# Kernel optimization log

Hardware: AMD Instinct MI355X
Metric: run time of the kernel (lower is better)

Reference implementation:

```python
import jax, jax.numpy as jnp
import numpy as np
from functools import partial

B, T, H, W, CIN, F = 8, 16, 64, 64, 32, 32
K = 3
BN_EPS = 1e-3


def _conv(x, w):
    # x: [N,H,W,Cin], w: [kh,kw,Cin,Cout], SAME padding, stride 1
    return jax.lax.conv_general_dilated(
        x, w, window_strides=(1, 1), padding='SAME',
        dimension_numbers=('NHWC', 'HWIO', 'NHWC'))


def _hard_sigmoid(x):
    # Keras hard_sigmoid: clip(0.2*x + 0.5, 0, 1)
    return jnp.clip(0.2 * x + 0.5, 0.0, 1.0)


def setup_inputs() -> dict:
    key = jax.random.key(0)
    ks = jax.random.split(key, 4)
    x = jax.random.normal(ks[0], (B, T, H, W, CIN), dtype=jnp.float32)
    Wx = jax.random.normal(ks[1], (K, K, CIN, 4 * F), dtype=jnp.float32) * 0.05
    Wh = jax.random.normal(ks[2], (K, K, F, 4 * F), dtype=jnp.float32) * 0.05
    b = jnp.zeros((4 * F,), dtype=jnp.float32)
    gamma = jnp.ones((F,), dtype=jnp.float32)
    beta = jnp.zeros((F,), dtype=jnp.float32)
    moving_mean = jnp.zeros((F,), dtype=jnp.float32)
    moving_var = jnp.ones((F,), dtype=jnp.float32)
    return {"x": x, "Wx": Wx, "Wh": Wh, "b": b, "gamma": gamma,
            "beta": beta, "moving_mean": moving_mean, "moving_var": moving_var}


def _conv_lstm(x, Wx, Wh, b):
    # Precompute input-to-gate convs for all timesteps at once: [B*T,H,W,4F]
    xg = _conv(x.reshape(B * T, H, W, CIN), Wx) + b
    xg = xg.reshape(B, T, H, W, 4 * F).transpose(1, 0, 2, 3, 4)  # [T,B,H,W,4F]

    def step(carry, xg_t):
        h, c = carry
        g = xg_t + _conv(h, Wh)  # [B,H,W,4F]
        i, f, cc, o = jnp.split(g, 4, axis=-1)  # Keras gate order i,f,c,o
        i = _hard_sigmoid(i)
        f = _hard_sigmoid(f)
        o = _hard_sigmoid(o)
        c = f * c + i * jnp.tanh(cc)
        h = o * jnp.tanh(c)
        return (h, c), h

    h0 = jnp.zeros((B, H, W, F), dtype=x.dtype)
    c0 = jnp.zeros((B, H, W, F), dtype=x.dtype)
    _, hs = jax.lax.scan(step, (h0, c0), xg)  # hs: [T,B,H,W,F]
    return hs.transpose(1, 0, 2, 3, 4)  # [B,T,H,W,F]


def reference(x, Wx, Wh, b, gamma, beta, moving_mean, moving_var):
    y = _conv_lstm(x, Wx, Wh, b)
    # BatchNorm in inference mode (training=False): use moving stats, eps=1e-3
    inv = gamma * jax.lax.rsqrt(moving_var + BN_EPS)
    return y * inv + (beta - moving_mean * inv)
```

## Files before the change

kernel.cpp:

```cpp
#include <hip/hip_runtime.h>
#include <math.h>

#define PSTR 40
#define GSTR 35
#define GPL  (64 * GSTR)

typedef _Float16 half8 __attribute__((ext_vector_type(8)));
typedef float    f32x4 __attribute__((ext_vector_type(4)));

__device__ __forceinline__ float fast_tanh(float v) {
    float e = __expf(2.f * v);
    return 1.f - 2.f / (e + 1.f);
}
__device__ __forceinline__ float hsig(float v) {
    return fminf(fmaxf(0.2f * v + 0.5f, 0.f), 1.f);
}

__global__ void prep_w(const float* __restrict__ Wx, const float* __restrict__ Wh,
                       _Float16* __restrict__ Wcx, _Float16* __restrict__ Wch) {
    const int k = blockIdx.x;
    const int n = threadIdx.x;
    const int tap = k >> 6, ci = k & 63;
    if (ci < 32) Wcx[(tap * 128 + n) * 32 + ci]        = (_Float16)Wx[(tap * 32 + ci) * 128 + n];
    else         Wch[(tap * 128 + n) * 32 + (ci - 32)] = (_Float16)Wh[(tap * 32 + (ci - 32)) * 128 + n];
}

__global__ __launch_bounds__(256, 2)
void lstm_step_k(const float* __restrict__ x, const _Float16* __restrict__ Wcx,
                 const _Float16* __restrict__ Wch, const float* __restrict__ bias,
                 const float* __restrict__ gamma_, const float* __restrict__ beta_,
                 const float* __restrict__ mmean, const float* __restrict__ mvar,
                 const _Float16* __restrict__ hprev, _Float16* __restrict__ hnext,
                 float* __restrict__ csw, float* __restrict__ out, int t)
{
    __shared__ _Float16 xp[100 * PSTR];
    __shared__ _Float16 hp[100 * PSTR];
    __shared__ float    glds[4 * GPL];

    const int tid  = threadIdx.x;
    const int lane = tid & 63;
    const int w    = tid >> 6;
    const int l15  = lane & 15, quad = lane >> 4;
    const int b = blockIdx.x, tx = blockIdx.y, ty = blockIdx.z;
    const int px0 = tx * 8, py0 = ty * 8;
    const int tile = ty * 8 + tx;

    const float* xt = x + (((size_t)b * 16 + t) * 4096) * 32;
    for (int i = tid; i < 400; i += 256) {
        const int pos = i >> 2, q = i & 3;
        const int row = pos / 10, col = pos - row * 10;
        const int gy = py0 + row - 1, gx = px0 + col - 1;
        half8 hv = {0, 0, 0, 0, 0, 0, 0, 0};
        if ((unsigned)gy < 64u && (unsigned)gx < 64u) {
            const float* s = xt + ((size_t)(gy * 64 + gx)) * 32 + q * 8;
            const float4 v0 = *(const float4*)s;
            const float4 v1 = *(const float4*)(s + 4);
            hv = (half8){(_Float16)v0.x, (_Float16)v0.y, (_Float16)v0.z, (_Float16)v0.w,
                         (_Float16)v1.x, (_Float16)v1.y, (_Float16)v1.z, (_Float16)v1.w};
        }
        *(half8*)&xp[pos * PSTR + q * 8] = hv;
    }
    if (t > 0) {
        const _Float16* hb = hprev + (size_t)b * 4096 * 32;
        for (int i = tid; i < 400; i += 256) {
            const int pos = i >> 2, q = i & 3;
            const int row = pos / 10, col = pos - row * 10;
            const int gy = py0 + row - 1, gx = px0 + col - 1;
            half8 hv = {0, 0, 0, 0, 0, 0, 0, 0};
            if ((unsigned)gy < 64u && (unsigned)gx < 64u)
                hv = *(const half8*)(hb + ((size_t)(gy * 64 + gx)) * 32 + q * 8);
            *(half8*)&hp[pos * PSTR + q * 8] = hv;
        }
    }

    const float bi0 = bias[w * 32 + l15];
    const float bi1 = bias[w * 32 + 16 + l15];

    __syncthreads();

    f32x4 acc[4][2];
    #pragma unroll
    for (int mt = 0; mt < 4; ++mt) {
        acc[mt][0] = (f32x4){bi0, bi0, bi0, bi0};
        acc[mt][1] = (f32x4){bi1, bi1, bi1, bi1};
    }

    int pb[4];
    #pragma unroll
    for (int mt = 0; mt < 4; ++mt) {
        const int p = mt * 16 + l15;
        pb[mt] = ((mt * 2 + (l15 >> 3)) * 10 + (l15 & 7)) * PSTR + quad * 8;
    }
    const _Float16* wbx = Wcx + ((size_t)(w * 32 + l15)) * 32 + quad * 8;
    const _Float16* wbh = Wch + ((size_t)(w * 32 + l15)) * 32 + quad * 8;

    #pragma unroll
    for (int tap = 0; tap < 9; ++tap) {
        const int ky = tap / 3, kx = tap - ky * 3;
        const int toff = (ky * 10 + kx) * PSTR;
        half8 a[4];
        #pragma unroll
        for (int mt = 0; mt < 4; ++mt) a[mt] = *(const half8*)&xp[pb[mt] + toff];
        #pragma unroll
        for (int ntl = 0; ntl < 2; ++ntl) {
            const half8 bf = *(const half8*)(wbx + tap * 4096 + ntl * 512);
            #pragma unroll
            for (int mt = 0; mt < 4; ++mt)
                acc[mt][ntl] = __builtin_amdgcn_mfma_f32_16x16x32_f16(a[mt], bf, acc[mt][ntl], 0, 0, 0);
        }
    }
    if (t > 0) {
        #pragma unroll
        for (int tap = 0; tap < 9; ++tap) {
            const int ky = tap / 3, kx = tap - ky * 3;
            const int toff = (ky * 10 + kx) * PSTR;
            half8 a[4];
            #pragma unroll
            for (int mt = 0; mt < 4; ++mt) a[mt] = *(const half8*)&hp[pb[mt] + toff];
            #pragma unroll
            for (int ntl = 0; ntl < 2; ++ntl) {
                const half8 bf = *(const half8*)(wbh + tap * 4096 + ntl * 512);
                #pragma unroll
                for (int mt = 0; mt < 4; ++mt)
                    acc[mt][ntl] = __builtin_amdgcn_mfma_f32_16x16x32_f16(a[mt], bf, acc[mt][ntl], 0, 0, 0);
            }
        }
    }

    #pragma unroll
    for (int mt = 0; mt < 4; ++mt)
        #pragma unroll
        for (int ntl = 0; ntl < 2; ++ntl)
            #pragma unroll
            for (int r = 0; r < 4; ++r) {
                const int px = mt * 16 + quad * 4 + r;
                glds[w * GPL + px * GSTR + ntl * 16 + l15] = acc[mt][ntl][r];
            }

    __syncthreads();

    const int pxt = tid >> 2, f0 = (tid & 3) * 8;
    const int gy = py0 + (pxt >> 3), gx = px0 + (pxt & 7);

    float gav[8], bev[8], mmv[8], mvv[8];
    *(float4*)&gav[0] = *(const float4*)&gamma_[f0];
    *(float4*)&gav[4] = *(const float4*)&gamma_[f0 + 4];
    *(float4*)&bev[0] = *(const float4*)&beta_[f0];
    *(float4*)&bev[4] = *(const float4*)&beta_[f0 + 4];
    *(float4*)&mmv[0] = *(const float4*)&mmean[f0];
    *(float4*)&mmv[4] = *(const float4*)&mmean[f0 + 4];
    *(float4*)&mvv[0] = *(const float4*)&mvar[f0];
    *(float4*)&mvv[4] = *(const float4*)&mvar[f0 + 4];

    float* cp = csw + (((size_t)b * 64 + tile) * 256 + tid) * 8;
    float cov[8];
    #pragma unroll
    for (int j = 0; j < 8; ++j) cov[j] = 0.f;
    if (t > 0) {
        *(f32x4*)&cov[0] = *(const f32x4*)cp;
        *(f32x4*)&cov[4] = *(const f32x4*)(cp + 4);
    }

    const int gb = pxt * GSTR + f0;
    half8 hv8;
    float ov[8], cnv[8];
    #pragma unroll
    for (int j = 0; j < 8; ++j) {
        const float gi = glds[0 * GPL + gb + j];
        const float gf = glds[1 * GPL + gb + j];
        const float gc = glds[2 * GPL + gb + j];
        const float go = glds[3 * GPL + gb + j];
        const float inv = gav[j] * rsqrtf(mvv[j] + 1e-3f);
        const float bnb = bev[j] - mmv[j] * inv;
        const float cn = hsig(gf) * cov[j] + hsig(gi) * fast_tanh(gc);
        const float hh = hsig(go) * fast_tanh(cn);
        cnv[j] = cn;
        hv8[j] = (_Float16)hh;
        ov[j] = hh * inv + bnb;
    }

    const size_t pix = ((size_t)(gy * 64 + gx)) * 32 + f0;
    _Float16* hq = hnext + (size_t)b * 4096 * 32;
    float* oq = out + (((size_t)b * 16 + t) * 4096) * 32;
    *(half8*)(hq + pix) = hv8;
    *(float4*)(oq + pix)     = *(float4*)&ov[0];
    *(float4*)(oq + pix + 4) = *(float4*)&ov[4];
    *(f32x4*)cp       = *(f32x4*)&cnv[0];
    *(f32x4*)(cp + 4) = *(f32x4*)&cnv[4];
}

extern "C" void kernel_launch(void* const* d_in, const int* in_sizes, int n_in,
                              void* d_out, int out_size, void* d_ws, size_t ws_size,
                              hipStream_t stream)
{
    const float* x      = (const float*)d_in[0];
    const float* Wx     = (const float*)d_in[1];
    const float* Wh     = (const float*)d_in[2];
    const float* bias   = (const float*)d_in[3];
    const float* gamma_ = (const float*)d_in[4];
    const float* beta_  = (const float*)d_in[5];
    const float* mmean  = (const float*)d_in[6];
    const float* mvar   = (const float*)d_in[7];
    float* out = (float*)d_out;

    char* wsb = (char*)d_ws;
    _Float16* h0  = (_Float16*)(wsb);
    _Float16* h1  = (_Float16*)(wsb + (1 << 21));
    float*    csw = (float*)(wsb + (1 << 22));
    _Float16* Wcx = (_Float16*)(wsb + (1 << 23));
    _Float16* Wch = (_Float16*)(wsb + (1 << 23) + 73728);

    prep_w<<<dim3(576), dim3(128), 0, stream>>>(Wx, Wh, Wcx, Wch);

    _Float16* hpr = h0;
    _Float16* hnx = h1;
    for (int t = 0; t < 16; ++t) {
        lstm_step_k<<<dim3(8, 8, 8), 256, 0, stream>>>(
            x, Wcx, Wch, bias, gamma_, beta_, mmean, mvar, hpr, hnx, csw, out, t);
        _Float16* tmp = hpr; hpr = hnx; hnx = tmp;
    }
}
```

Before: 293.0 us.

## Pre-convert x to fp16 and load conv operands directly from global memory

Adds a prep kernel that converts all of x to fp16 once, so each step reads half-precision input. The shared-memory halo staging and its barrier are dropped; every lane now loads its MFMA A-fragments straight from global memory (relying on L1/L2 caches) with per-tap bounds checks. The cell-state load is moved earlier to overlap with compute, and the h/c writes are skipped on the last timestep. The trade-off is 9x redundant global loads per tap and an extra full pass over x, in exchange for less LDS traffic, no staging barrier and higher potential occupancy.

```diff
diff --git a/kernel.cpp b/kernel.cpp
--- a/kernel.cpp
+++ b/kernel.cpp
@@ -1,7 +1,6 @@
 #include <hip/hip_runtime.h>
 #include <math.h>
 
-#define PSTR 40
 #define GSTR 35
 #define GPL  (64 * GSTR)
 
@@ -25,17 +24,24 @@
     else         Wch[(tap * 128 + n) * 32 + (ci - 32)] = (_Float16)Wh[(tap * 32 + (ci - 32)) * 128 + n];
 }
 
+__global__ __launch_bounds__(256)
+void prep_x(const float* __restrict__ x, _Float16* __restrict__ x16) {
+    const size_t i = ((size_t)blockIdx.x * 256 + threadIdx.x) * 8;
+    const float4 v0 = *(const float4*)(x + i);
+    const float4 v1 = *(const float4*)(x + i + 4);
+    *(half8*)(x16 + i) = (half8){(_Float16)v0.x, (_Float16)v0.y, (_Float16)v0.z, (_Float16)v0.w,
+                                 (_Float16)v1.x, (_Float16)v1.y, (_Float16)v1.z, (_Float16)v1.w};
+}
+
 __global__ __launch_bounds__(256, 2)
-void lstm_step_k(const float* __restrict__ x, const _Float16* __restrict__ Wcx,
+void lstm_step_k(const _Float16* __restrict__ x16, const _Float16* __restrict__ Wcx,
                  const _Float16* __restrict__ Wch, const float* __restrict__ bias,
                  const float* __restrict__ gamma_, const float* __restrict__ beta_,
                  const float* __restrict__ mmean, const float* __restrict__ mvar,
                  const _Float16* __restrict__ hprev, _Float16* __restrict__ hnext,
                  float* __restrict__ csw, float* __restrict__ out, int t)
 {
-    __shared__ _Float16 xp[100 * PSTR];
-    __shared__ _Float16 hp[100 * PSTR];
-    __shared__ float    glds[4 * GPL];
+    __shared__ float glds[4 * GPL];
 
     const int tid  = threadIdx.x;
     const int lane = tid & 63;
@@ -45,38 +51,25 @@
     const int px0 = tx * 8, py0 = ty * 8;
     const int tile = ty * 8 + tx;
 
-    const float* xt = x + (((size_t)b * 16 + t) * 4096) * 32;
-    for (int i = tid; i < 400; i += 256) {
-        const int pos = i >> 2, q = i & 3;
-        const int row = pos / 10, col = pos - row * 10;
-        const int gy = py0 + row - 1, gx = px0 + col - 1;
-        half8 hv = {0, 0, 0, 0, 0, 0, 0, 0};
-        if ((unsigned)gy < 64u && (unsigned)gx < 64u) {
-            const float* s = xt + ((size_t)(gy * 64 + gx)) * 32 + q * 8;
-            const float4 v0 = *(const float4*)s;
-            const float4 v1 = *(const float4*)(s + 4);
-            hv = (half8){(_Float16)v0.x, (_Float16)v0.y, (_Float16)v0.z, (_Float16)v0.w,
-                         (_Float16)v1.x, (_Float16)v1.y, (_Float16)v1.z, (_Float16)v1.w};
-        }
-        *(half8*)&xp[pos * PSTR + q * 8] = hv;
-    }
+    const int c0 = l15 & 7;
+    int rowm[4];
+    #pragma unroll
+    for (int mt = 0; mt < 4; ++mt) rowm[mt] = mt * 2 + (l15 >> 3);
+
+    const _Float16* xb = x16 + ((size_t)(b * 16 + t) * 4096) * 32;
+    const _Float16* hb = hprev + (size_t)b * 4096 * 32;
+
+    float* cp = csw + (((size_t)b * 64 + tile) * 256 + tid) * 8;
+    float cov[8];
+    #pragma unroll
+    for (int j = 0; j < 8; ++j) cov[j] = 0.f;
     if (t > 0) {
-        const _Float16* hb = hprev + (size_t)b * 4096 * 32;
-        for (int i = tid; i < 400; i += 256) {
-            const int pos = i >> 2, q = i & 3;
-            const int row = pos / 10, col = pos - row * 10;
-            const int gy = py0 + row - 1, gx = px0 + col - 1;
-            half8 hv = {0, 0, 0, 0, 0, 0, 0, 0};
-            if ((unsigned)gy < 64u && (unsigned)gx < 64u)
-                hv = *(const half8*)(hb + ((size_t)(gy * 64 + gx)) * 32 + q * 8);
-            *(half8*)&hp[pos * PSTR + q * 8] = hv;
-        }
+        *(f32x4*)&cov[0] = *(const f32x4*)cp;
+        *(f32x4*)&cov[4] = *(const f32x4*)(cp + 4);
     }
 
     const float bi0 = bias[w * 32 + l15];
     const float bi1 = bias[w * 32 + 16 + l15];
-
-    __syncthreads();
 
     f32x4 acc[4][2];
     #pragma unroll
@@ -85,22 +78,22 @@
         acc[mt][1] = (f32x4){bi1, bi1, bi1, bi1};
     }
 
-    int pb[4];
-    #pragma unroll
-    for (int mt = 0; mt < 4; ++mt) {
-        const int p = mt * 16 + l15;
-        pb[mt] = ((mt * 2 + (l15 >> 3)) * 10 + (l15 & 7)) * PSTR + quad * 8;
-    }
     const _Float16* wbx = Wcx + ((size_t)(w * 32 + l15)) * 32 + quad * 8;
     const _Float16* wbh = Wch + ((size_t)(w * 32 + l15)) * 32 + quad * 8;
 
     #pragma unroll
     for (int tap = 0; tap < 9; ++tap) {
         const int ky = tap / 3, kx = tap - ky * 3;
-        const int toff = (ky * 10 + kx) * PSTR;
+        const int gx = px0 + c0 + kx - 1;
+        const bool vx = (unsigned)gx < 64u;
         half8 a[4];
         #pragma unroll
-        for (int mt = 0; mt < 4; ++mt) a[mt] = *(const half8*)&xp[pb[mt] + toff];
+        for (int mt = 0; mt < 4; ++mt) {
+            const int gy = py0 + rowm[mt] + ky - 1;
+            a[mt] = (half8){0, 0, 0, 0, 0, 0, 0, 0};
+            if (vx && (unsigned)gy < 64u)
+                a[mt] = *(const half8*)(xb + ((size_t)(gy * 64 + gx)) * 32 + quad * 8);
+        }
         #pragma unroll
         for (int ntl = 0; ntl < 2; ++ntl) {
             const half8 bf = *(const half8*)(wbx + tap * 4096 + ntl * 512);
@@ -113,10 +106,16 @@
         #pragma unroll
         for (int tap = 0; tap < 9; ++tap) {
             const int ky = tap / 3, kx = tap - ky * 3;
-            const int toff = (ky * 10 + kx) * PSTR;
+            const int gx = px0 + c0 + kx - 1;
+            const bool vx = (unsigned)gx < 64u;
             half8 a[4];
             #pragma unroll
-            for (int mt = 0; mt < 4; ++mt) a[mt] = *(const half8*)&hp[pb[mt] + toff];
+            for (int mt = 0; mt < 4; ++mt) {
+                const int gy = py0 + rowm[mt] + ky - 1;
+                a[mt] = (half8){0, 0, 0, 0, 0, 0, 0, 0};
+                if (vx && (unsigned)gy < 64u)
+                    a[mt] = *(const half8*)(hb + ((size_t)(gy * 64 + gx)) * 32 + quad * 8);
+            }
             #pragma unroll
             for (int ntl = 0; ntl < 2; ++ntl) {
                 const half8 bf = *(const half8*)(wbh + tap * 4096 + ntl * 512);
@@ -151,15 +150,6 @@
     *(float4*)&mmv[4] = *(const float4*)&mmean[f0 + 4];
     *(float4*)&mvv[0] = *(const float4*)&mvar[f0];
     *(float4*)&mvv[4] = *(const float4*)&mvar[f0 + 4];
-
-    float* cp = csw + (((size_t)b * 64 + tile) * 256 + tid) * 8;
-    float cov[8];
-    #pragma unroll
-    for (int j = 0; j < 8; ++j) cov[j] = 0.f;
-    if (t > 0) {
-        *(f32x4*)&cov[0] = *(const f32x4*)cp;
-        *(f32x4*)&cov[4] = *(const f32x4*)(cp + 4);
-    }
 
     const int gb = pxt * GSTR + f0;
     half8 hv8;
@@ -180,13 +170,15 @@
     }
 
     const size_t pix = ((size_t)(gy * 64 + gx)) * 32 + f0;
-    _Float16* hq = hnext + (size_t)b * 4096 * 32;
     float* oq = out + (((size_t)b * 16 + t) * 4096) * 32;
-    *(half8*)(hq + pix) = hv8;
     *(float4*)(oq + pix)     = *(float4*)&ov[0];
     *(float4*)(oq + pix + 4) = *(float4*)&ov[4];
-    *(f32x4*)cp       = *(f32x4*)&cnv[0];
-    *(f32x4*)(cp + 4) = *(f32x4*)&cnv[4];
+    if (t < 15) {
+        _Float16* hq = hnext + (size_t)b * 4096 * 32;
+        *(half8*)(hq + pix) = hv8;
+        *(f32x4*)cp       = *(f32x4*)&cnv[0];
+        *(f32x4*)(cp + 4) = *(f32x4*)&cnv[4];
+    }
 }
 
 extern "C" void kernel_launch(void* const* d_in, const int* in_sizes, int n_in,
@@ -207,16 +199,18 @@
     _Float16* h0  = (_Float16*)(wsb);
     _Float16* h1  = (_Float16*)(wsb + (1 << 21));
     float*    csw = (float*)(wsb + (1 << 22));
-    _Float16* Wcx = (_Float16*)(wsb + (1 << 23));
-    _Float16* Wch = (_Float16*)(wsb + (1 << 23) + 73728);
+    _Float16* x16 = (_Float16*)(wsb + (1 << 23));
+    _Float16* Wcx = (_Float16*)(wsb + (1 << 23) + (1 << 25));
+    _Float16* Wch = (_Float16*)(wsb + (1 << 23) + (1 << 25) + 73728);
 
     prep_w<<<dim3(576), dim3(128), 0, stream>>>(Wx, Wh, Wcx, Wch);
+    prep_x<<<dim3(8192), dim3(256), 0, stream>>>(x, x16);
 
     _Float16* hpr = h0;
     _Float16* hnx = h1;
     for (int t = 0; t < 16; ++t) {
         lstm_step_k<<<dim3(8, 8, 8), 256, 0, stream>>>(
-            x, Wcx, Wch, bias, gamma_, beta_, mmean, mvar, hpr, hnx, csw, out, t);
+            x16, Wcx, Wch, bias, gamma_, beta_, mmean, mvar, hpr, hnx, csw, out, t);
         _Float16* tmp = hpr; hpr = hnx; hnx = tmp;
     }
 }
```

After: 392.3 us. +33.9%, slower.
